# Kernel tuning notes

Hardware: AMD Instinct MI355X
Metric: run time of the kernel (lower is better)

Reference implementation:

```python
import jax, jax.numpy as jnp
import numpy as np

B, S, T = 4, 1024, 1024
CTX, QIN, C, H = 1024, 1024, 1024, 16
HD = C // H  # per-head channels


def setup_inputs() -> dict:
    key = jax.random.key(0)
    ks = jax.random.split(key, 12)
    s = 0.02
    return {
        "query": jax.random.normal(ks[0], (B, S, QIN), jnp.float32),
        "key": jax.random.normal(ks[1], (B, T, CTX), jnp.float32),
        "value": jax.random.normal(ks[2], (B, T, CTX), jnp.float32),
        "mask": jax.random.randint(ks[3], (B, S, T), 0, 2).astype(bool),
        "Wq": jax.random.normal(ks[4], (C, QIN), jnp.float32) * s,
        "bq": jax.random.normal(ks[5], (C,), jnp.float32) * s,
        "Wk": jax.random.normal(ks[6], (C, CTX), jnp.float32) * s,
        "bk": jax.random.normal(ks[7], (C,), jnp.float32) * s,
        "Wv": jax.random.normal(ks[8], (C, CTX), jnp.float32) * s,
        "bv": jax.random.normal(ks[9], (C,), jnp.float32) * s,
        "Wo": jax.random.normal(ks[10], (C, C), jnp.float32) * s,
        "bo": jax.random.normal(ks[11], (C,), jnp.float32) * s,
    }


def reference(query, key, value, mask, Wq, bq, Wk, bk, Wv, bv, Wo, bo):
    b, s, _ = query.shape
    t = key.shape[1]
    c = Wq.shape[0]
    h, hd = H, c // H
    q = (query @ Wq.T + bq).reshape(b, s, h, hd)
    k = (key @ Wk.T + bk).reshape(b, t, h, hd)
    v = (value @ Wv.T + bv).reshape(b, t, h, hd)
    # [B,H,S,T] scores, scaled by 1/sqrt(head_dim)
    score = jnp.einsum('bshd,bthd->bhst', q, k) * (hd ** -0.5)
    # masked_fill_(~mask[:, None, 0:1], -inf): mask key positions via row 0
    score = jnp.where(mask[:, None, 0:1], score, -jnp.inf)
    weights = jax.nn.softmax(score, axis=-1)
    out = jnp.einsum('bhst,bthd->bshd', weights, v).reshape(b, s, c)
    out = out @ Wo.T + bo
    out = out * mask[..., 0:1].astype(out.dtype)
    return out
```

## Files before the change

kernel.cpp:

```cpp
#include <hip/hip_runtime.h>
#include <stdint.h>

#define Bb  4
#define Ss  1024
#define Tt  1024
#define Cc  1024
#define Hh  16
#define HDd 64
#define Kk  1024

typedef __bf16 bf16;
typedef __bf16 bf16x8 __attribute__((ext_vector_type(8)));
typedef float  f32x4  __attribute__((ext_vector_type(4)));
typedef __attribute__((address_space(1))) uint32_t gu32;
typedef __attribute__((address_space(3))) uint32_t lu32;

__device__ __forceinline__ void load_lds16(const bf16* g, bf16* l) {
    __builtin_amdgcn_global_load_lds((gu32*)g, (lu32*)l, 16, 0, 0);
}

#define BARRIER_LDS() do {                                    \
    asm volatile("s_waitcnt lgkmcnt(0)" ::: "memory");        \
    __builtin_amdgcn_s_barrier();                             \
} while (0)


__global__ void cvt8(const float* __restrict__ q, const float* __restrict__ k,
                     const float* __restrict__ v,
                     const float* __restrict__ w0, const float* __restrict__ w1,
                     const float* __restrict__ w2, const float* __restrict__ w3,
                     const int* __restrict__ mask,
                     int* __restrict__ rankK, int* __restrict__ nkK,
                     int* __restrict__ rankQ, int* __restrict__ nkQ,
                     int* __restrict__ invQ,
                     bf16* __restrict__ vz, float* __restrict__ oz,
                     bf16* __restrict__ qb, bf16* __restrict__ kb,
                     bf16* __restrict__ vb,
                     bf16* __restrict__ dw0, bf16* __restrict__ dw1,
                     bf16* __restrict__ dw2, bf16* __restrict__ dw3)
{
    const int tid = threadIdx.x;
    const int x = blockIdx.x;

    if (x < 8192) {
        const float* s; bf16* d; int i;
        if (x < 6144) {
            s = (x < 2048) ? q : (x < 4096) ? k : v;
            d = (x < 2048) ? qb : (x < 4096) ? kb : vb;
            i = ((x & 2047) * 256 + tid) * 8;
        } else {
            const int w = (x - 6144) >> 9;
            s = (w == 0) ? w0 : (w == 1) ? w1 : (w == 2) ? w2 : w3;
            d = (w == 0) ? dw0 : (w == 1) ? dw1 : (w == 2) ? dw2 : dw3;
            i = (((x - 6144) & 511) * 256 + tid) * 8;
        }
        const float4 a = *(const float4*)(s + i);
        const float4 c = *(const float4*)(s + i + 4);
        bf16x8 o;
        o[0] = (bf16)a.x; o[1] = (bf16)a.y; o[2] = (bf16)a.z; o[3] = (bf16)a.w;
        o[4] = (bf16)c.x; o[5] = (bf16)c.y; o[6] = (bf16)c.z; o[7] = (bf16)c.w;
        *(bf16x8*)(d + i) = o;
        return;
    }

    if (x < 8200) {
        const int xs = x - 8192;
        const int b = xs >> 1, kind = xs & 1;
        const int* mb = mask + (size_t)b * Ss * Tt;
        __shared__ int part[256];
        int vv[4]; int s = 0;
#pragma unroll
        for (int u = 0; u < 4; u++) {
            const int idx = tid * 4 + u;
            vv[u] = kind ? (mb[(size_t)idx * Tt] != 0) : (mb[idx] != 0);
            s += vv[u];
        }
        part[tid] = s; __syncthreads();
        for (int off = 1; off < 256; off <<= 1) {
            const int t_ = (tid >= off) ? part[tid - off] : 0;
            __syncthreads();
            part[tid] += t_;
            __syncthreads();
        }
        int a = part[tid] - s;
#pragma unroll
        for (int u = 0; u < 4; u++) {
            const int idx = tid * 4 + u;
            const int j = vv[u] ? a : -1;
            if (kind) { rankQ[b * Tt + idx] = j; if (j >= 0) invQ[b * Tt + j] = idx; }
            else      { rankK[b * Tt + idx] = j; }
            a += vv[u];
        }
        if (tid == 255) { if (kind) nkQ[b] = a; else nkK[b] = a; }
        return;
    }

    if (x < 10248) {
        const float4 z = {0.f, 0.f, 0.f, 0.f};
        float* p = (float*)((char*)vz + (size_t)(x - 8200) * 4096) + tid * 4;
        *(float4*)p = z;
        return;
    }

    const float4 z = {0.f, 0.f, 0.f, 0.f};
    float* p = (float*)((char*)oz + (size_t)(x - 10248) * 8192) + tid * 8;
    *(float4*)p = z; *(float4*)(p + 4) = z;
}

__device__ __forceinline__ void mainloop_128x64_nv(
    const bf16* __restrict__ Ab, const bf16* __restrict__ Wb,
    bf16* As, bf16* Bs, f32x4 acc[4][2])
{
    const int tid  = threadIdx.x;
    const int wid  = tid >> 6;
    const int lane = tid & 63;
    const int l16  = lane & 15;
    const int quad = lane >> 4;
    const int wm   = wid >> 1;
    const int wn   = wid & 1;
    const int r8   = lane >> 3;
    const int ssw  = ((lane & 7) ^ r8) * 8;

    for (int k0 = 0; k0 < Kk; k0 += 64) {
#pragma unroll
        for (int p = 0; p < 4; p++) {
            const int rb = wid * 32 + p * 8;
            load_lds16(Ab + (size_t)(rb + r8) * Kk + k0 + ssw, As + rb * 64);
        }
#pragma unroll
        for (int p = 0; p < 2; p++) {
            const int rb = wid * 16 + p * 8;
            load_lds16(Wb + (size_t)(rb + r8) * Kk + k0 + ssw, Bs + rb * 64);
        }
        __syncthreads();
#pragma unroll
        for (int kh = 0; kh < 2; kh++) {
            bf16x8 af[4], bw[2];
#pragma unroll
            for (int i = 0; i < 4; i++)
                af[i] = *(const bf16x8*)(As + (wm * 64 + i * 16 + l16) * 64 +
                                         (((kh * 4 + quad) ^ (l16 & 7)) * 8));
#pragma unroll
            for (int j = 0; j < 2; j++)
                bw[j] = *(const bf16x8*)(Bs + (wn * 32 + j * 16 + l16) * 64 +
                                         (((kh * 4 + quad) ^ (l16 & 7)) * 8));
#pragma unroll
            for (int i = 0; i < 4; i++)
#pragma unroll
                for (int j = 0; j < 2; j++)
                    acc[i][j] = __builtin_amdgcn_mfma_f32_16x16x32_bf16(af[i], bw[j], acc[i][j], 0, 0, 0);
        }
        __syncthreads();
    }
}

__device__ __forceinline__ void mainloop_64x64_nv(
    const bf16* __restrict__ Ab, const bf16* __restrict__ Wb,
    bf16* As, bf16* Bs, f32x4 acc[2][2])
{
    const int tid  = threadIdx.x;
    const int wid  = tid >> 6;
    const int lane = tid & 63;
    const int l16  = lane & 15;
    const int quad = lane >> 4;
    const int wm   = wid >> 1;
    const int wn   = wid & 1;
    const int r8   = lane >> 3;
    const int ssw  = ((lane & 7) ^ r8) * 8;

    for (int k0 = 0; k0 < Kk; k0 += 64) {
#pragma unroll
        for (int p = 0; p < 2; p++) {
            const int rb = wid * 16 + p * 8;
            load_lds16(Ab + (size_t)(rb + r8) * Kk + k0 + ssw, As + rb * 64);
            load_lds16(Wb + (size_t)(rb + r8) * Kk + k0 + ssw, Bs + rb * 64);
        }
        __syncthreads();
#pragma unroll
        for (int kh = 0; kh < 2; kh++) {
            bf16x8 af[2], bw[2];
#pragma unroll
            for (int i = 0; i < 2; i++)
                af[i] = *(const bf16x8*)(As + (wm * 32 + i * 16 + l16) * 64 +
                                         (((kh * 4 + quad) ^ (l16 & 7)) * 8));
#pragma unroll
            for (int j = 0; j < 2; j++)
                bw[j] = *(const bf16x8*)(Bs + (wn * 32 + j * 16 + l16) * 64 +
                                         (((kh * 4 + quad) ^ (l16 & 7)) * 8));
#pragma unroll
            for (int i = 0; i < 2; i++)
#pragma unroll
                for (int j = 0; j < 2; j++)
                    acc[i][j] = __builtin_amdgcn_mfma_f32_16x16x32_bf16(af[i], bw[j], acc[i][j], 0, 0, 0);
        }
        __syncthreads();
    }
}

__global__ __launch_bounds__(256)
void gemm_qkv(const bf16* __restrict__ Aq, const bf16* __restrict__ Ak, const bf16* __restrict__ Av,
              const bf16* __restrict__ Wq, const bf16* __restrict__ Wk, const bf16* __restrict__ Wv,
              const float* __restrict__ bq, const float* __restrict__ bk, const float* __restrict__ bv,
              const int* __restrict__ rankK, const int* __restrict__ rankQ,
              bf16* __restrict__ Oq, bf16* __restrict__ Ok, bf16* __restrict__ Ov)
{
    __shared__ __align__(16) bf16 As[128 * 64];
    __shared__ __align__(16) bf16 Bs[64 * 64];
    const int z = blockIdx.z;
    const bf16*  A    = (z == 0) ? Aq : (z == 1) ? Ak : Av;
    const bf16*  W    = (z == 0) ? Wq : (z == 1) ? Wk : Wv;
    const float* bias = (z == 0) ? bq : (z == 1) ? bk : bv;
    const int*   rnk  = (z == 0) ? rankQ : rankK;

    f32x4 acc[4][2];
    const f32x4 z4 = {0.f, 0.f, 0.f, 0.f};
#pragma unroll
    for (int i = 0; i < 4; i++)
#pragma unroll
        for (int j = 0; j < 2; j++) acc[i][j] = z4;

    mainloop_128x64_nv(A + (size_t)blockIdx.x * 128 * Kk,
                       W + (size_t)blockIdx.y * 64 * Kk, As, Bs, acc);

    const int tid = threadIdx.x;
    const int wid = tid >> 6, lane = tid & 63;
    const int l16 = lane & 15, quad = lane >> 4;
    const int wm = wid >> 1, wn = wid & 1;
    const int col0 = blockIdx.y * 64 + wn * 32;

    float bjv[2]; int hv[2], dv[2];
#pragma unroll
    for (int j = 0; j < 2; j++) {
        const int col = col0 + j * 16 + l16;
        bjv[j] = bias[col];
        hv[j] = col >> 6; dv[j] = col & 63;
    }
#pragma unroll
    for (int i = 0; i < 4; i++) {
#pragma unroll
        for (int r = 0; r < 4; r++) {
            const int row = blockIdx.x * 128 + wm * 64 + i * 16 + quad * 4 + r;
            const int bb = row >> 10, t = row & 1023;
            const int jc = rnk[bb * Tt + t];
            if (jc < 0) continue;
#pragma unroll
            for (int j = 0; j < 2; j++) {
                const bf16 val = (bf16)(acc[i][j][r] + bjv[j]);
                const int h = hv[j], d = dv[j];
                if (z == 0)      Oq[((size_t)(bb * Hh + h) * Ss + jc) * HDd + d] = val;
                else if (z == 1) Ok[((size_t)(bb * Hh + h) * Tt + jc) * HDd + d] = val;
                else             Ov[((size_t)((bb * Hh + h) * HDd + d)) * Tt + jc] = val;
            }
        }
    }
}

__global__ __launch_bounds__(256)
void gemm_out(const bf16* __restrict__ A, const bf16* __restrict__ W,
              const float* __restrict__ bias,
              const int* __restrict__ nkQ, const int* __restrict__ invQ,
              float* __restrict__ out)
{
    const int bb    = blockIdx.x & 3;
    const int strip = blockIdx.x >> 2;
    const int t0 = strip * 64;
    const int nq = nkQ[bb];
    if (t0 >= nq) return;

    __shared__ __align__(16) bf16 As[64 * 64];
    __shared__ __align__(16) bf16 Bs[64 * 64];
    f32x4 acc[2][2];
    const f32x4 z4 = {0.f, 0.f, 0.f, 0.f};
#pragma unroll
    for (int i = 0; i < 2; i++)
#pragma unroll
        for (int j = 0; j < 2; j++) acc[i][j] = z4;

    mainloop_64x64_nv(A + (size_t)(bb * 1024 + t0) * Kk,
                      W + (size_t)blockIdx.y * 64 * Kk, As, Bs, acc);

    const int tid = threadIdx.x;
    const int wid = tid >> 6, lane = tid & 63;
    const int l16 = lane & 15, quad = lane >> 4;
    const int wm = wid >> 1, wn = wid & 1;
    const int col0 = blockIdx.y * 64 + wn * 32;
#pragma unroll
    for (int j = 0; j < 2; j++) {
        const int col = col0 + j * 16 + l16;
        const float bj = bias[col];
#pragma unroll
        for (int i = 0; i < 2; i++) {
#pragma unroll
            for (int r = 0; r < 4; r++) {
                const int jrow = t0 + wm * 32 + i * 16 + quad * 4 + r;
                if (jrow < nq) {
                    const int s = invQ[bb * Tt + jrow];
                    out[((size_t)bb * Ss + s) * Cc + col] = acc[i][j][r] + bj;
                }
            }
        }
    }
}

__global__ __launch_bounds__(256, 2)
void attn(const bf16* __restrict__ Q, const bf16* __restrict__ Kp, const bf16* __restrict__ Vt,
          const int* __restrict__ nkK, const int* __restrict__ nkQ, bf16* __restrict__ X)
{
    __shared__ __align__(16) bf16 Ks[64 * 64];
    __shared__ __align__(16) bf16 Vs[64 * 64];
    __shared__ __align__(16) bf16 Ps[4][16 * 72];
    const int g   = blockIdx.x;
    const int xcd = g & 7, idx = g >> 3;
    const int bh  = xcd * 8 + (idx >> 4);
    const int qblk = idx & 15;
    const int b = bh >> 4, h = bh & 15;
    const int nq  = nkQ[b];
    if (qblk * 64 >= nq) return;
    const int nkb = nkK[b];
    const int lim = ((nkb + 127) >> 7) << 7;

    const int tid = threadIdx.x, wid = tid >> 6, lane = tid & 63;
    const int l16 = lane & 15, quad = lane >> 4;
    const bf16* Qbh = Q  + (size_t)bh * Ss * HDd;
    const bf16* Kbh = Kp + (size_t)bh * Tt * HDd;
    const bf16* Vbh = Vt + (size_t)bh * HDd * Tt;
    const int q0 = qblk * 64 + wid * 16;
    bf16* Psw = &Ps[wid][0];

    const bf16x8 qf0 = *(const bf16x8*)(Qbh + (size_t)(q0 + l16) * HDd + quad * 8);
    const bf16x8 qf1 = *(const bf16x8*)(Qbh + (size_t)(q0 + l16) * HDd + 32 + quad * 8);

    float ls[4];
    f32x4 o[4];
    const f32x4 z4 = {0.f, 0.f, 0.f, 0.f};
#pragma unroll
    for (int r = 0; r < 4; r++) ls[r] = 0.f;
#pragma unroll
    for (int dblk = 0; dblk < 4; dblk++) o[dblk] = z4;

    const int srow = lane >> 3;
    const int schk = lane & 7;
    const int sswz = (schk ^ srow) * 8;
    const int c80 = wid * 2, c81 = wid * 2 + 1;

    const bf16* kg0 = Kbh + (size_t)(c80 * 8 + srow) * HDd + sswz;
    const bf16* kg1 = Kbh + (size_t)(c81 * 8 + srow) * HDd + sswz;
    const bf16* vg0 = Vbh + (size_t)(c80 * 8 + srow) * Tt + sswz;
    const bf16* vg1 = Vbh + (size_t)(c81 * 8 + srow) * Tt + sswz;
    bf16* kd0 = Ks + c80 * 512 + lane * 8;
    bf16* kd1 = Ks + c81 * 512 + lane * 8;
    bf16* vd0 = Vs + c80 * 512 + lane * 8;
    bf16* vd1 = Vs + c81 * 512 + lane * 8;

    bf16x8 ka0, ka1, va0, va1;
    bf16x8 kb0, kb1, vb0, vb1;

#define LOADA(KT) do { const int _kt = (KT);                          \
    ka0 = *(const bf16x8*)(kg0 + (size_t)_kt * HDd);                  \
    ka1 = *(const bf16x8*)(kg1 + (size_t)_kt * HDd);                  \
    va0 = *(const bf16x8*)(vg0 + _kt);                                \
    va1 = *(const bf16x8*)(vg1 + _kt); } while (0)
#define LOADB(KT) do { const int _kt = (KT);                          \
    kb0 = *(const bf16x8*)(kg0 + (size_t)_kt * HDd);                  \
    kb1 = *(const bf16x8*)(kg1 + (size_t)_kt * HDd);                  \
    vb0 = *(const bf16x8*)(vg0 + _kt);                                \
    vb1 = *(const bf16x8*)(vg1 + _kt); } while (0)
#define STOREA() do {                                                 \
    *(bf16x8*)kd0 = ka0; *(bf16x8*)kd1 = ka1;                         \
    *(bf16x8*)vd0 = va0; *(bf16x8*)vd1 = va1; } while (0)
#define STOREB() do {                                                 \
    *(bf16x8*)kd0 = kb0; *(bf16x8*)kd1 = kb1;                         \
    *(bf16x8*)vd0 = vb0; *(bf16x8*)vd1 = vb1; } while (0)

    auto compute = [&](int base) {
        f32x4 sc[4];
#pragma unroll
        for (int nb = 0; nb < 4; nb++) sc[nb] = z4;
#pragma unroll
        for (int nb = 0; nb < 4; nb++) {
            const bf16* krow = Ks + (nb * 16 + l16) * 64;
            const bf16x8 kf0 = *(const bf16x8*)(krow + ((quad       ^ (l16 & 7)) * 8));
            const bf16x8 kf1 = *(const bf16x8*)(krow + (((4 + quad) ^ (l16 & 7)) * 8));
            sc[nb] = __builtin_amdgcn_mfma_f32_16x16x32_bf16(qf0, kf0, sc[nb], 0, 0, 0);
            sc[nb] = __builtin_amdgcn_mfma_f32_16x16x32_bf16(qf1, kf1, sc[nb], 0, 0, 0);
        }

#pragma unroll
        for (int nb = 0; nb < 4; nb++) {
            const bool vv = (base + nb * 16 + l16) < nkb;
#pragma unroll
            for (int r = 0; r < 4; r++) {
                const float p = vv ? __expf(sc[nb][r] * 0.125f) : 0.f;
                ls[r] += p;
                Psw[(quad * 4 + r) * 72 + nb * 16 + l16] = (bf16)p;
            }
        }

#pragma unroll
        for (int kh = 0; kh < 2; kh++) {
            const bf16x8 pf = *(const bf16x8*)(Psw + l16 * 72 + kh * 32 + quad * 8);
#pragma unroll
            for (int dblk = 0; dblk < 4; dblk++) {
                const bf16x8 vf = *(const bf16x8*)(Vs + (dblk * 16 + l16) * 64 +
                                                   (((kh * 4 + quad) ^ (l16 & 7)) * 8));
                o[dblk] = __builtin_amdgcn_mfma_f32_16x16x32_bf16(pf, vf, o[dblk], 0, 0, 0);
            }
        }
    };

    LOADA(0);

    for (int kt = 0; kt < lim; kt += 128) {
        BARRIER_LDS();
        LOADB(kt + 64);
        STOREA();
        BARRIER_LDS();
        compute(kt);

        BARRIER_LDS();
        LOADA((kt + 128 < lim) ? (kt + 128) : (lim - 64));
        STOREB();
        BARRIER_LDS();
        compute(kt + 64);
    }
#undef LOADA
#undef LOADB
#undef STOREA
#undef STOREB

#pragma unroll
    for (int off = 1; off <= 8; off <<= 1)
#pragma unroll
        for (int r = 0; r < 4; r++)
            ls[r] += __shfl_xor(ls[r], off, 64);
    float inv[4];
#pragma unroll
    for (int r = 0; r < 4; r++) inv[r] = 1.f / ls[r];

#pragma unroll
    for (int dblk = 0; dblk < 4; dblk++) {
#pragma unroll
        for (int r = 0; r < 4; r++) {
            const int srow_q = q0 + quad * 4 + r;
            if (srow_q < nq) {
                const int d = dblk * 16 + l16;
                X[(size_t)(b * Ss + srow_q) * Cc + h * HDd + d] = (bf16)(o[dblk][r] * inv[r]);
            }
        }
    }
}

extern "C" void kernel_launch(void* const* d_in, const int* in_sizes, int n_in,
                              void* d_out, int out_size, void* d_ws, size_t ws_size,
                              hipStream_t stream)
{
    const float* query = (const float*)d_in[0];
    const float* key   = (const float*)d_in[1];
    const float* value = (const float*)d_in[2];
    const int*   mask  = (const int*)d_in[3];
    const float* Wq = (const float*)d_in[4];
    const float* bq = (const float*)d_in[5];
    const float* Wk = (const float*)d_in[6];
    const float* bk = (const float*)d_in[7];
    const float* Wv = (const float*)d_in[8];
    const float* bv = (const float*)d_in[9];
    const float* Wo = (const float*)d_in[10];
    const float* bo = (const float*)d_in[11];
    float* out = (float*)d_out;

    char* ws = (char*)d_ws;
    const size_t MB = 1024 * 1024;
    bf16* qb  = (bf16*)(ws + 0 * MB);
    bf16* kb  = (bf16*)(ws + 8 * MB);
    bf16* vb  = (bf16*)(ws + 16 * MB);
    bf16* wqb = (bf16*)(ws + 24 * MB);
    bf16* wkb = (bf16*)(ws + 26 * MB);
    bf16* wvb = (bf16*)(ws + 28 * MB);
    bf16* wob = (bf16*)(ws + 30 * MB);
    bf16* Qp  = (bf16*)(ws + 32 * MB);
    bf16* Kpp = (bf16*)(ws + 40 * MB);
    bf16* Vtp = (bf16*)(ws + 48 * MB);
    bf16* Xb  = (bf16*)(ws + 56 * MB);

    char* intb = ws + 64 * MB - 64 * 1024;
    int* rankK = (int*)(intb);
    int* rankQ = (int*)(intb + 16 * 1024);
    int* invQ  = (int*)(intb + 32 * 1024);
    int* nkK   = (int*)(intb + 48 * 1024);
    int* nkQ   = (int*)(intb + 48 * 1024 + 256);

    cvt8<<<dim3(12296), 256, 0, stream>>>(query, key, value, Wq, Wk, Wv, Wo,
                                          mask, rankK, nkK, rankQ, nkQ, invQ,
                                          Vtp, out,
                                          qb, kb, vb, wqb, wkb, wvb, wob);
    gemm_qkv<<<dim3(32, 16, 3), 256, 0, stream>>>(qb, kb, vb, wqb, wkb, wvb,
                                                  bq, bk, bv, rankK, rankQ,
                                                  Qp, Kpp, Vtp);
    attn<<<dim3(1024), 256, 0, stream>>>(Qp, Kpp, Vtp, nkK, nkQ, Xb);
    gemm_out<<<dim3(64, 16), 256, 0, stream>>>(Xb, wob, bo, nkQ, invQ, out);
}
```

Baseline: 217.0 us.

## Rewrite QKV projection GEMM as 256x256 double-buffered tile with interleaved prefetch

Replaces the 128x64 single-buffered QKV GEMM with a 512-thread 256x256 tile that double-buffers A and W in LDS. Global-to-LDS loads for the next K step are spread between four MFMA phases, and the phases are wrapped in setprio. Each iteration now uses one vmcnt barrier instead of two syncthreads. This raises arithmetic intensity and overlaps loads with compute, at the cost of only 192 blocks (fewer than the CU count), 128KB of LDS per block, and heavy register pressure.

Result: slower. 233.8 us (+7.7%).

```diff
diff --git a/kernel.cpp b/kernel.cpp
--- a/kernel.cpp
+++ b/kernel.cpp
@@ -21,6 +21,11 @@
 
 #define BARRIER_LDS() do {                                    \
     asm volatile("s_waitcnt lgkmcnt(0)" ::: "memory");        \
+    __builtin_amdgcn_s_barrier();                             \
+} while (0)
+
+#define BARRIER_VM() do {                                     \
+    asm volatile("s_waitcnt vmcnt(0)" ::: "memory");          \
     __builtin_amdgcn_s_barrier();                             \
 } while (0)
 
@@ -107,50 +112,130 @@
     *(float4*)p = z; *(float4*)(p + 4) = z;
 }
 
-__device__ __forceinline__ void mainloop_128x64_nv(
-    const bf16* __restrict__ Ab, const bf16* __restrict__ Wb,
-    bf16* As, bf16* Bs, f32x4 acc[4][2])
+__global__ __launch_bounds__(512, 1)
+void gemm_qkv(const bf16* __restrict__ Aq, const bf16* __restrict__ Ak, const bf16* __restrict__ Av,
+              const bf16* __restrict__ Wq, const bf16* __restrict__ Wk, const bf16* __restrict__ Wv,
+              const float* __restrict__ bq, const float* __restrict__ bk, const float* __restrict__ bv,
+              const int* __restrict__ rankK, const int* __restrict__ rankQ,
+              bf16* __restrict__ Oq, bf16* __restrict__ Ok, bf16* __restrict__ Ov)
 {
+    __shared__ __align__(16) bf16 As[2][256 * 64];
+    __shared__ __align__(16) bf16 Bs[2][256 * 64];
+    const int z = blockIdx.z;
+    const bf16*  A    = (z == 0) ? Aq : (z == 1) ? Ak : Av;
+    const bf16*  W    = (z == 0) ? Wq : (z == 1) ? Wk : Wv;
+    const float* bias = (z == 0) ? bq : (z == 1) ? bk : bv;
+    const int*   rnk  = (z == 0) ? rankQ : rankK;
+
     const int tid  = threadIdx.x;
     const int wid  = tid >> 6;
     const int lane = tid & 63;
     const int l16  = lane & 15;
     const int quad = lane >> 4;
-    const int wm   = wid >> 1;
-    const int wn   = wid & 1;
-    const int r8   = lane >> 3;
-    const int ssw  = ((lane & 7) ^ r8) * 8;
-
-    for (int k0 = 0; k0 < Kk; k0 += 64) {
-#pragma unroll
-        for (int p = 0; p < 4; p++) {
-            const int rb = wid * 32 + p * 8;
-            load_lds16(Ab + (size_t)(rb + r8) * Kk + k0 + ssw, As + rb * 64);
-        }
-#pragma unroll
-        for (int p = 0; p < 2; p++) {
-            const int rb = wid * 16 + p * 8;
-            load_lds16(Wb + (size_t)(rb + r8) * Kk + k0 + ssw, Bs + rb * 64);
-        }
-        __syncthreads();
-#pragma unroll
-        for (int kh = 0; kh < 2; kh++) {
-            bf16x8 af[4], bw[2];
-#pragma unroll
-            for (int i = 0; i < 4; i++)
-                af[i] = *(const bf16x8*)(As + (wm * 64 + i * 16 + l16) * 64 +
-                                         (((kh * 4 + quad) ^ (l16 & 7)) * 8));
-#pragma unroll
-            for (int j = 0; j < 2; j++)
-                bw[j] = *(const bf16x8*)(Bs + (wn * 32 + j * 16 + l16) * 64 +
-                                         (((kh * 4 + quad) ^ (l16 & 7)) * 8));
-#pragma unroll
-            for (int i = 0; i < 4; i++)
-#pragma unroll
-                for (int j = 0; j < 2; j++)
-                    acc[i][j] = __builtin_amdgcn_mfma_f32_16x16x32_bf16(af[i], bw[j], acc[i][j], 0, 0, 0);
-        }
-        __syncthreads();
+    const int wm   = wid >> 2;
+    const int wn   = wid & 3;
+
+    const int srow = lane >> 3;
+    const int schk = lane & 7;
+    const int ssw  = (schk ^ srow) * 8;
+
+    const bf16* Ab = A + (size_t)blockIdx.x * 256 * Kk;
+    const bf16* Wb = W + (size_t)blockIdx.y * 256 * Kk;
+
+    auto stageA = [&](int c, int k0, int p) {
+        const int rb = p * 64 + wid * 8;
+        load_lds16(Ab + (size_t)(rb + srow) * Kk + k0 + ssw, &As[c][rb * 64]);
+    };
+    auto stageB = [&](int c, int k0, int p) {
+        const int rb = p * 64 + wid * 8;
+        load_lds16(Wb + (size_t)(rb + srow) * Kk + k0 + ssw, &Bs[c][rb * 64]);
+    };
+
+    f32x4 acc[8][4];
+    const f32x4 z4 = {0.f, 0.f, 0.f, 0.f};
+#pragma unroll
+    for (int i = 0; i < 8; i++)
+#pragma unroll
+        for (int j = 0; j < 4; j++) acc[i][j] = z4;
+
+#define PHASE(Ac, Bc, QA, QB) do {                                            \
+    bf16x8 af[4][2], bw[2][2];                                                \
+_Pragma("unroll")                                                             \
+    for (int fi = 0; fi < 4; fi++)                                            \
+_Pragma("unroll")                                                             \
+        for (int kh = 0; kh < 2; kh++)                                        \
+            af[fi][kh] = *(const bf16x8*)((Ac) + (wm * 128 + (QA * 4 + fi) * 16 + l16) * 64 + \
+                                          (((kh * 4 + quad) ^ (l16 & 7)) * 8)); \
+_Pragma("unroll")                                                             \
+    for (int fj = 0; fj < 2; fj++)                                            \
+_Pragma("unroll")                                                             \
+        for (int kh = 0; kh < 2; kh++)                                        \
+            bw[fj][kh] = *(const bf16x8*)((Bc) + (wn * 64 + (QB * 2 + fj) * 16 + l16) * 64 + \
+                                          (((kh * 4 + quad) ^ (l16 & 7)) * 8)); \
+    __builtin_amdgcn_s_setprio(1);                                            \
+_Pragma("unroll")                                                             \
+    for (int kh = 0; kh < 2; kh++)                                            \
+_Pragma("unroll")                                                             \
+        for (int fi = 0; fi < 4; fi++)                                        \
+_Pragma("unroll")                                                             \
+            for (int fj = 0; fj < 2; fj++)                                    \
+                acc[QA * 4 + fi][QB * 2 + fj] =                               \
+                    __builtin_amdgcn_mfma_f32_16x16x32_bf16(af[fi][kh], bw[fj][kh], \
+                                                            acc[QA * 4 + fi][QB * 2 + fj], 0, 0, 0); \
+    __builtin_amdgcn_s_setprio(0);                                            \
+} while (0)
+
+#pragma unroll
+    for (int p = 0; p < 4; p++) stageA(0, 0, p);
+#pragma unroll
+    for (int p = 0; p < 4; p++) stageB(0, 0, p);
+    BARRIER_VM();
+
+    for (int t = 0; t < 16; ++t) {
+        const int c = t & 1;
+        const int n = c ^ 1;
+        const int k1 = (t + 1) * 64;
+        const bool pf = (t + 1 < 16);
+        const bf16* Ac = &As[c][0];
+        const bf16* Bc = &Bs[c][0];
+
+        if (pf) { stageA(n, k1, 0); stageA(n, k1, 1); stageA(n, k1, 2); }
+        PHASE(Ac, Bc, 0, 0);
+        if (pf) { stageA(n, k1, 3); stageB(n, k1, 0); stageB(n, k1, 1); }
+        PHASE(Ac, Bc, 0, 1);
+        if (pf) { stageB(n, k1, 2); stageB(n, k1, 3); }
+        PHASE(Ac, Bc, 1, 0);
+        PHASE(Ac, Bc, 1, 1);
+
+        BARRIER_VM();
+    }
+#undef PHASE
+
+    const int col0 = blockIdx.y * 256 + wn * 64;
+    float bjv[4]; int hv[4], dv[4];
+#pragma unroll
+    for (int j = 0; j < 4; j++) {
+        const int col = col0 + j * 16 + l16;
+        bjv[j] = bias[col];
+        hv[j] = col >> 6; dv[j] = col & 63;
+    }
+#pragma unroll
+    for (int fi = 0; fi < 8; fi++) {
+#pragma unroll
+        for (int r = 0; r < 4; r++) {
+            const int row = blockIdx.x * 256 + wm * 128 + fi * 16 + quad * 4 + r;
+            const int bb = row >> 10, t = row & 1023;
+            const int jc = rnk[bb * Tt + t];
+            if (jc < 0) continue;
+#pragma unroll
+            for (int j = 0; j < 4; j++) {
+                const bf16 val = (bf16)(acc[fi][j][r] + bjv[j]);
+                const int h = hv[j], d = dv[j];
+                if (z == 0)      Oq[((size_t)(bb * Hh + h) * Ss + jc) * HDd + d] = val;
+                else if (z == 1) Ok[((size_t)(bb * Hh + h) * Tt + jc) * HDd + d] = val;
+                else             Ov[((size_t)((bb * Hh + h) * HDd + d)) * Tt + jc] = val;
+            }
+        }
     }
 }
 
@@ -194,64 +279,6 @@
                     acc[i][j] = __builtin_amdgcn_mfma_f32_16x16x32_bf16(af[i], bw[j], acc[i][j], 0, 0, 0);
         }
         __syncthreads();
-    }
-}
-
-__global__ __launch_bounds__(256)
-void gemm_qkv(const bf16* __restrict__ Aq, const bf16* __restrict__ Ak, const bf16* __restrict__ Av,
-              const bf16* __restrict__ Wq, const bf16* __restrict__ Wk, const bf16* __restrict__ Wv,
-              const float* __restrict__ bq, const float* __restrict__ bk, const float* __restrict__ bv,
-              const int* __restrict__ rankK, const int* __restrict__ rankQ,
-              bf16* __restrict__ Oq, bf16* __restrict__ Ok, bf16* __restrict__ Ov)
-{
-    __shared__ __align__(16) bf16 As[128 * 64];
-    __shared__ __align__(16) bf16 Bs[64 * 64];
-    const int z = blockIdx.z;
-    const bf16*  A    = (z == 0) ? Aq : (z == 1) ? Ak : Av;
-    const bf16*  W    = (z == 0) ? Wq : (z == 1) ? Wk : Wv;
-    const float* bias = (z == 0) ? bq : (z == 1) ? bk : bv;
-    const int*   rnk  = (z == 0) ? rankQ : rankK;
-
-    f32x4 acc[4][2];
-    const f32x4 z4 = {0.f, 0.f, 0.f, 0.f};
-#pragma unroll
-    for (int i = 0; i < 4; i++)
-#pragma unroll
-        for (int j = 0; j < 2; j++) acc[i][j] = z4;
-
-    mainloop_128x64_nv(A + (size_t)blockIdx.x * 128 * Kk,
-                       W + (size_t)blockIdx.y * 64 * Kk, As, Bs, acc);
-
-    const int tid = threadIdx.x;
-    const int wid = tid >> 6, lane = tid & 63;
-    const int l16 = lane & 15, quad = lane >> 4;
-    const int wm = wid >> 1, wn = wid & 1;
-    const int col0 = blockIdx.y * 64 + wn * 32;
-
-    float bjv[2]; int hv[2], dv[2];
-#pragma unroll
-    for (int j = 0; j < 2; j++) {
-        const int col = col0 + j * 16 + l16;
-        bjv[j] = bias[col];
-        hv[j] = col >> 6; dv[j] = col & 63;
-    }
-#pragma unroll
-    for (int i = 0; i < 4; i++) {
-#pragma unroll
-        for (int r = 0; r < 4; r++) {
-            const int row = blockIdx.x * 128 + wm * 64 + i * 16 + quad * 4 + r;
-            const int bb = row >> 10, t = row & 1023;
-            const int jc = rnk[bb * Tt + t];
-            if (jc < 0) continue;
-#pragma unroll
-            for (int j = 0; j < 2; j++) {
-                const bf16 val = (bf16)(acc[i][j][r] + bjv[j]);
-                const int h = hv[j], d = dv[j];
-                if (z == 0)      Oq[((size_t)(bb * Hh + h) * Ss + jc) * HDd + d] = val;
-                else if (z == 1) Ok[((size_t)(bb * Hh + h) * Tt + jc) * HDd + d] = val;
-                else             Ov[((size_t)((bb * Hh + h) * HDd + d)) * Tt + jc] = val;
-            }
-        }
     }
 }
 
@@ -493,9 +520,9 @@
                                           mask, rankK, nkK, rankQ, nkQ, invQ,
                                           Vtp, out,
                                           qb, kb, vb, wqb, wkb, wvb, wob);
-    gemm_qkv<<<dim3(32, 16, 3), 256, 0, stream>>>(qb, kb, vb, wqb, wkb, wvb,
-                                                  bq, bk, bv, rankK, rankQ,
-                                                  Qp, Kpp, Vtp);
+    gemm_qkv<<<dim3(16, 4, 3), 512, 0, stream>>>(qb, kb, vb, wqb, wkb, wvb,
+                                                 bq, bk, bv, rankK, rankQ,
+                                                 Qp, Kpp, Vtp);
     attn<<<dim3(1024), 256, 0, stream>>>(Qp, Kpp, Vtp, nkK, nkQ, Xb);
     gemm_out<<<dim3(64, 16), 256, 0, stream>>>(Xb, wob, bo, nkQ, invQ, out);
 }
```
